# Performance work log

Hardware: AMD Instinct MI355X
Metric: run time of the kernel (lower is better)

The kernel has to match this reference:

```python
import jax, jax.numpy as jnp
import numpy as np

B, L, H, O, T = 64, 128, 1024, 1, 256


def setup_inputs() -> dict:
    key = jax.random.key(0)
    ks = jax.random.split(key, 9)
    s = 1.0 / np.sqrt(H)
    return {
        "latent": jax.random.normal(ks[0], (B, L), dtype=jnp.float32),
        "W_lin": jax.random.normal(ks[1], (H, L), dtype=jnp.float32) / np.sqrt(L),
        "b_lin": jax.random.normal(ks[2], (H,), dtype=jnp.float32) * 0.01,
        "W_ih": jax.random.normal(ks[3], (4 * H, H), dtype=jnp.float32) * s,
        "W_hh": jax.random.normal(ks[4], (4 * H, H), dtype=jnp.float32) * s,
        "b_ih": jax.random.normal(ks[5], (4 * H,), dtype=jnp.float32) * s,
        "b_hh": jax.random.normal(ks[6], (4 * H,), dtype=jnp.float32) * s,
        "W_out": jax.random.normal(ks[7], (O, H), dtype=jnp.float32) / np.sqrt(H),
        "b_out": jax.random.normal(ks[8], (O,), dtype=jnp.float32) * 0.01,
        "seq_len": T,
    }


def reference(latent, W_lin, b_lin, W_ih, W_hh, b_ih, b_hh, W_out, b_out, seq_len):
    # latent -> hidden projection: [B, H]
    hidden = latent @ W_lin.T + b_lin
    h_dim = W_hh.shape[1]
    batch = hidden.shape[0]
    # Input is identical at every timestep, so the input-to-gate projection
    # is computed once (same math as applying it per step). [B, 4H]
    x_gates = hidden @ W_ih.T + (b_ih + b_hh)

    def step(carry, _):
        h, c = carry
        gates = x_gates + h @ W_hh.T  # [B, 4H]
        i, f, g, o = jnp.split(gates, 4, axis=-1)  # PyTorch gate order i,f,g,o
        i = jax.nn.sigmoid(i)
        f = jax.nn.sigmoid(f)
        g = jnp.tanh(g)
        o = jax.nn.sigmoid(o)
        c = f * c + i * g
        h = o * jnp.tanh(c)
        return (h, c), h

    init = (jnp.zeros((batch, h_dim), hidden.dtype), jnp.zeros((batch, h_dim), hidden.dtype))
    _, hs = jax.lax.scan(step, init, None, length=seq_len)  # [T, B, H]
    decoded = jnp.transpose(hs, (1, 0, 2))  # [B, T, H]
    out = decoded @ W_out.T + b_out  # [B, T, O]
    return out
```

## Files before the change

kernel.cpp:

```cpp
#include <hip/hip_runtime.h>
#include <hip/hip_cooperative_groups.h>

#define B_  64
#define L_  128
#define H_  1024
#define G4_ 4096
#define T_  256
#define NWG 256

typedef __attribute__((ext_vector_type(8))) short bf16x8;
typedef __attribute__((ext_vector_type(4))) float f32x4;

__device__ __forceinline__ float shx(float v, int m) { return __shfl_xor(v, m, 64); }

__device__ __forceinline__ unsigned rne_bf16(float x) {
    unsigned u = __builtin_bit_cast(unsigned, x);
    return (u + 0x7FFFu + ((u >> 16) & 1u)) >> 16;
}
__device__ __forceinline__ float bf16_to_f32(unsigned h) {
    return __builtin_bit_cast(float, h << 16);
}

__global__ void hidden_kernel(const float* __restrict__ latent,
                              const float* __restrict__ W_lin,
                              const float* __restrict__ b_lin,
                              float* __restrict__ hidden) {
    const int wave = (blockIdx.x * blockDim.x + threadIdx.x) >> 6;
    const int lane = threadIdx.x & 63;
    for (int o = 0; o < 64; ++o) {
        const int out = wave * 64 + o;
        const int b = out >> 10, j = out & 1023;
        const float2 wv = *(const float2*)(W_lin + j * L_ + lane * 2);
        const float2 xv = *(const float2*)(latent + b * L_ + lane * 2);
        float p = wv.x * xv.x + wv.y * xv.y;
        #pragma unroll
        for (int m = 1; m < 64; m <<= 1) p += shx(p, m);
        if (lane == 0) hidden[out] = p + b_lin[j];
    }
}

__global__ void xgates_kernel(const float* __restrict__ hidden,
                              const float* __restrict__ W_ih,
                              const float* __restrict__ b_ih,
                              const float* __restrict__ b_hh,
                              float* __restrict__ x_gates) {
    const int wave = (blockIdx.x * blockDim.x + threadIdx.x) >> 6;
    const int lane = threadIdx.x & 63;
    for (int o = 0; o < 64; ++o) {
        const int out = wave * 64 + o;
        const int b = out >> 12, j = out & 4095;
        float p = 0.f;
        #pragma unroll
        for (int q = 0; q < 4; ++q) {
            const float4 wv = *(const float4*)(W_ih + j * H_ + q * 256 + lane * 4);
            const float4 hv = *(const float4*)(hidden + b * H_ + q * 256 + lane * 4);
            p += wv.x * hv.x + wv.y * hv.y + wv.z * hv.z + wv.w * hv.w;
        }
        #pragma unroll
        for (int m = 1; m < 64; m <<= 1) p += shx(p, m);
        if (lane == 0) x_gates[out] = p + b_ih[j] + b_hh[j];
    }
}

__global__ void __launch_bounds__(1024, 4)
lstm_kernel(const float* __restrict__ W_hh,
            const float* __restrict__ x_gates,
            const float* __restrict__ W_out,
            unsigned* __restrict__ h_buf,
            float* __restrict__ part,
            int*   __restrict__ bar)
{
    extern __shared__ float smem[];
    unsigned* Hhi32 = (unsigned*)smem;
    unsigned* Hlo32 = (unsigned*)smem + 8192;
    float*    Gred  = smem + 16384;

    const int tid = threadIdx.x;
    const int l   = tid & 63;
    const int wv  = tid >> 6;
    const int tau = wv & 3;
    const int kq  = wv >> 2;
    const int hs  = blockIdx.x >> 2;
    const int bg  = blockIdx.x & 3;
    const int row16 = l & 15;
    const int kg    = l >> 4;

    bf16x8 Ahi[8], Alo[8];
    {
        const float* wrow = W_hh + (size_t)(tau * H_ + hs * 16 + row16) * H_;
        #pragma unroll
        for (int s = 0; s < 8; ++s) {
            const int ks = kq * 8 + s;
            const float* p = wrow + ks * 32 + kg * 8;
            const float4 f0 = *(const float4*)p;
            const float4 f1 = *(const float4*)(p + 4);
            const float w[8] = {f0.x, f0.y, f0.z, f0.w, f1.x, f1.y, f1.z, f1.w};
            #pragma unroll
            for (int j = 0; j < 8; ++j) {
                const unsigned hb = rne_bf16(w[j]);
                const float lo = w[j] - bf16_to_f32(hb);
                Ahi[s][j] = (short)hb;
                Alo[s][j] = (short)rne_bf16(lo);
            }
        }
    }

    const int bb  = tid >> 4;
    const int hix = tid & 15;
    const int bG  = bg * 16 + bb;
    float xgi = 0, xgf = 0, xgg = 0, xgo = 0, wo = 0;
    if (tid < 256) {
        const float* xg = x_gates + (size_t)bG * G4_ + hs * 16 + hix;
        xgi = xg[0]; xgf = xg[H_]; xgg = xg[2 * H_]; xgo = xg[3 * H_];
        wo  = W_out[hs * 16 + hix];
    }
    float c_state = 0.f;

    int* cnt = bar + bg * 64;
    int* gen = bar + bg * 64 + 32;

    int cur = 0;
    for (int t = 0; t < T_; ++t) {
        {
            const int b = wv;
            const unsigned long long* src =
                (const unsigned long long*)(h_buf + (size_t)cur * (B_ * H_) +
                                            (size_t)(bg * 16 + b) * H_);
            #pragma unroll
            for (int i = 0; i < 8; ++i) {
                const int d = i * 64 + l;
                const unsigned long long v =
                    __hip_atomic_load(src + d, __ATOMIC_RELAXED,
                                      __HIP_MEMORY_SCOPE_AGENT);
                const unsigned p0 = (unsigned)v;
                const unsigned p1 = (unsigned)(v >> 32);
                const int dw = b * 512 + (((d >> 2) ^ (b & 7)) << 2) + (d & 3);
                Hhi32[dw] = (p1 & 0xFFFF0000u) | (p0 >> 16);
                Hlo32[dw] = ((p1 & 0xFFFFu) << 16) | (p0 & 0xFFFFu);
            }
        }
        __syncthreads();

        {
            f32x4 acc = {0.f, 0.f, 0.f, 0.f};
            const char* HhiB = (const char*)smem;
            const char* HloB = (const char*)smem + 32768;
            #pragma unroll
            for (int s = 0; s < 8; ++s) {
                const int ks  = kq * 8 + s;
                const int off = row16 * 2048 + (((ks * 4 + kg) ^ (row16 & 7)) << 4);
                const bf16x8 Bhi = *(const bf16x8*)(HhiB + off);
                const bf16x8 Blo = *(const bf16x8*)(HloB + off);
                acc = __builtin_amdgcn_mfma_f32_16x16x32_bf16(Ahi[s], Bhi, acc, 0, 0, 0);
                acc = __builtin_amdgcn_mfma_f32_16x16x32_bf16(Ahi[s], Blo, acc, 0, 0, 0);
                acc = __builtin_amdgcn_mfma_f32_16x16x32_bf16(Alo[s], Bhi, acc, 0, 0, 0);
            }
            #pragma unroll
            for (int r = 0; r < 4; ++r)
                Gred[((tau * 4 + kq) * 16 + kg * 4 + r) * 17 + row16] = acc[r];
        }
        __syncthreads();

        if (tid < 256) {
            float gs[4];
            #pragma unroll
            for (int g = 0; g < 4; ++g) {
                float s = 0.f;
                #pragma unroll
                for (int q = 0; q < 4; ++q)
                    s += Gred[((g * 4 + q) * 16 + hix) * 17 + bb];
                gs[g] = s;
            }
            const float gi_ = xgi + gs[0];
            const float gf_ = xgf + gs[1];
            const float gg_ = xgg + gs[2];
            const float go_ = xgo + gs[3];
            const float i_ = 1.f / (1.f + expf(-gi_));
            const float f_ = 1.f / (1.f + expf(-gf_));
            const float g_ = tanhf(gg_);
            const float o_ = 1.f / (1.f + expf(-go_));
            c_state = f_ * c_state + i_ * g_;
            const float hv = o_ * tanhf(c_state);
            const unsigned hb = rne_bf16(hv);
            const float lo = hv - bf16_to_f32(hb);
            const unsigned packed = (hb << 16) | rne_bf16(lo);
            __hip_atomic_store(h_buf + (size_t)(cur ^ 1) * (B_ * H_) +
                               (size_t)bG * H_ + hs * 16 + hix,
                               packed, __ATOMIC_RELAXED, __HIP_MEMORY_SCOPE_AGENT);
            float pp = hv * wo;
            pp += shx(pp, 1); pp += shx(pp, 2); pp += shx(pp, 4); pp += shx(pp, 8);
            if (hix == 0) part[((size_t)t * B_ + bG) * 64 + hs] = pp;
        }

        asm volatile("s_waitcnt vmcnt(0)" ::: "memory");
        __syncthreads();
        if (tid == 0) {
            if (__hip_atomic_fetch_add(cnt, 1, __ATOMIC_RELAXED,
                                       __HIP_MEMORY_SCOPE_AGENT) == 64 * (t + 1) - 1) {
                __hip_atomic_store(gen, t + 1, __ATOMIC_RELAXED,
                                   __HIP_MEMORY_SCOPE_AGENT);
            } else {
                while (__hip_atomic_load(gen, __ATOMIC_RELAXED,
                                         __HIP_MEMORY_SCOPE_AGENT) < t + 1) {}
            }
        }
        __syncthreads();
        cur ^= 1;
    }
}

__global__ void out_kernel(const float* __restrict__ part,
                           const float* __restrict__ b_out,
                           float* __restrict__ out) {
    const int g = blockIdx.x * blockDim.x + threadIdx.x;
    const int t = g >> 6, b = g & 63;
    const float4* p4 = (const float4*)(part + ((size_t)t * B_ + b) * 64);
    float s = 0.f;
    #pragma unroll
    for (int i = 0; i < 16; ++i) {
        const float4 v = p4[i];
        s += v.x + v.y + v.z + v.w;
    }
    out[b * T_ + t] = s + b_out[0];
}

extern "C" void kernel_launch(void* const* d_in, const int* in_sizes, int n_in,
                              void* d_out, int out_size, void* d_ws, size_t ws_size,
                              hipStream_t stream) {
    const float* latent = (const float*)d_in[0];
    const float* W_lin  = (const float*)d_in[1];
    const float* b_lin  = (const float*)d_in[2];
    const float* W_ih   = (const float*)d_in[3];
    const float* W_hh   = (const float*)d_in[4];
    const float* b_ih   = (const float*)d_in[5];
    const float* b_hh   = (const float*)d_in[6];
    const float* W_out  = (const float*)d_in[7];
    const float* b_out  = (const float*)d_in[8];

    float* ws      = (float*)d_ws;
    float* hidden  = ws;
    float* x_gates = hidden  + 65536;
    unsigned* h_buf = (unsigned*)(x_gates + 262144);
    float* part    = (float*)(h_buf + 131072);
    int*   bar     = (int*)(part + 1048576);
    float* out     = (float*)d_out;

    hipMemsetAsync(h_buf, 0, (size_t)2 * B_ * H_ * sizeof(unsigned), stream);
    hipMemsetAsync(bar, 0, 4 * 64 * sizeof(int), stream);

    const int lds_bytes = 65536 + 4352 * 4;
    hipFuncSetAttribute((const void*)lstm_kernel,
                        hipFuncAttributeMaxDynamicSharedMemorySize, lds_bytes);

    hidden_kernel<<<256, 256, 0, stream>>>(latent, W_lin, b_lin, hidden);
    xgates_kernel<<<1024, 256, 0, stream>>>(hidden, W_ih, b_ih, b_hh, x_gates);

    void* args[] = { (void*)&W_hh, (void*)&x_gates, (void*)&W_out,
                     (void*)&h_buf, (void*)&part, (void*)&bar };
    hipLaunchCooperativeKernel(reinterpret_cast<void*>(lstm_kernel),
                               dim3(NWG), dim3(1024), args, lds_bytes, stream);

    out_kernel<<<64, 256, 0, stream>>>(part, b_out, out);
}
```

Before: 1.767 ms.

## Replace counter barrier with per-block flags, store raw h in LDS, split gates per wave

```diff
diff --git a/kernel.cpp b/kernel.cpp
--- a/kernel.cpp
+++ b/kernel.cpp
@@ -1,5 +1,4 @@
 #include <hip/hip_runtime.h>
-#include <hip/hip_cooperative_groups.h>
 
 #define B_  64
 #define L_  128
@@ -10,6 +9,7 @@
 
 typedef __attribute__((ext_vector_type(8))) short bf16x8;
 typedef __attribute__((ext_vector_type(4))) float f32x4;
+typedef __attribute__((ext_vector_type(4))) unsigned u32x4;
 
 __device__ __forceinline__ float shx(float v, int m) { return __shfl_xor(v, m, 64); }
 
@@ -46,8 +46,8 @@
                               float* __restrict__ x_gates) {
     const int wave = (blockIdx.x * blockDim.x + threadIdx.x) >> 6;
     const int lane = threadIdx.x & 63;
-    for (int o = 0; o < 64; ++o) {
-        const int out = wave * 64 + o;
+    for (int o = 0; o < 16; ++o) {
+        const int out = wave * 16 + o;
         const int b = out >> 12, j = out & 4095;
         float p = 0.f;
         #pragma unroll
@@ -62,7 +62,7 @@
     }
 }
 
-__global__ void __launch_bounds__(1024, 4)
+__global__ void __launch_bounds__(1024, 2)
 lstm_kernel(const float* __restrict__ W_hh,
             const float* __restrict__ x_gates,
             const float* __restrict__ W_out,
@@ -71,26 +71,27 @@
             int*   __restrict__ bar)
 {
     extern __shared__ float smem[];
-    unsigned* Hhi32 = (unsigned*)smem;
-    unsigned* Hlo32 = (unsigned*)smem + 8192;
-    float*    Gred  = smem + 16384;
+    unsigned* Hraw = (unsigned*)smem;
+    float*    Gred = smem + 16384;
 
     const int tid = threadIdx.x;
     const int l   = tid & 63;
     const int wv  = tid >> 6;
-    const int tau = wv & 3;
-    const int kq  = wv >> 2;
+    const int kq  = wv >> 1;
+    const int tp  = wv & 1;
     const int hs  = blockIdx.x >> 2;
     const int bg  = blockIdx.x & 3;
     const int row16 = l & 15;
     const int kg    = l >> 4;
 
-    bf16x8 Ahi[8], Alo[8];
-    {
-        const float* wrow = W_hh + (size_t)(tau * H_ + hs * 16 + row16) * H_;
-        #pragma unroll
-        for (int s = 0; s < 8; ++s) {
-            const int ks = kq * 8 + s;
+    bf16x8 Ahi[2][4], Alo[2][4];
+    #pragma unroll
+    for (int g = 0; g < 2; ++g) {
+        const int gate = tp * 2 + g;
+        const float* wrow = W_hh + (size_t)(gate * H_ + hs * 16 + row16) * H_;
+        #pragma unroll
+        for (int s = 0; s < 4; ++s) {
+            const int ks = kq * 4 + s;
             const float* p = wrow + ks * 32 + kg * 8;
             const float4 f0 = *(const float4*)p;
             const float4 f1 = *(const float4*)(p + 4);
@@ -99,8 +100,8 @@
             for (int j = 0; j < 8; ++j) {
                 const unsigned hb = rne_bf16(w[j]);
                 const float lo = w[j] - bf16_to_f32(hb);
-                Ahi[s][j] = (short)hb;
-                Alo[s][j] = (short)rne_bf16(lo);
+                Ahi[g][s][j] = (short)hb;
+                Alo[g][s][j] = (short)rne_bf16(lo);
             }
         }
     }
@@ -116,48 +117,56 @@
     }
     float c_state = 0.f;
 
-    int* cnt = bar + bg * 64;
-    int* gen = bar + bg * 64 + 32;
-
+    unsigned long long* H64 = (unsigned long long*)Hraw;
     int cur = 0;
     for (int t = 0; t < T_; ++t) {
         {
-            const int b = wv;
             const unsigned long long* src =
                 (const unsigned long long*)(h_buf + (size_t)cur * (B_ * H_) +
-                                            (size_t)(bg * 16 + b) * H_);
+                                            (size_t)(bg * 16 + wv) * H_);
+            unsigned long long v[8];
+            #pragma unroll
+            for (int i = 0; i < 8; ++i)
+                v[i] = __hip_atomic_load(src + i * 64 + l, __ATOMIC_RELAXED,
+                                         __HIP_MEMORY_SCOPE_AGENT);
             #pragma unroll
             for (int i = 0; i < 8; ++i) {
                 const int d = i * 64 + l;
-                const unsigned long long v =
-                    __hip_atomic_load(src + d, __ATOMIC_RELAXED,
-                                      __HIP_MEMORY_SCOPE_AGENT);
-                const unsigned p0 = (unsigned)v;
-                const unsigned p1 = (unsigned)(v >> 32);
-                const int dw = b * 512 + (((d >> 2) ^ (b & 7)) << 2) + (d & 3);
-                Hhi32[dw] = (p1 & 0xFFFF0000u) | (p0 >> 16);
-                Hlo32[dw] = ((p1 & 0xFFFFu) << 16) | (p0 & 0xFFFFu);
+                H64[wv * 512 + (((d >> 1) ^ (wv & 7)) << 1) + (d & 1)] = v[i];
             }
         }
         __syncthreads();
 
         {
-            f32x4 acc = {0.f, 0.f, 0.f, 0.f};
-            const char* HhiB = (const char*)smem;
-            const char* HloB = (const char*)smem + 32768;
-            #pragma unroll
-            for (int s = 0; s < 8; ++s) {
-                const int ks  = kq * 8 + s;
-                const int off = row16 * 2048 + (((ks * 4 + kg) ^ (row16 & 7)) << 4);
-                const bf16x8 Bhi = *(const bf16x8*)(HhiB + off);
-                const bf16x8 Blo = *(const bf16x8*)(HloB + off);
-                acc = __builtin_amdgcn_mfma_f32_16x16x32_bf16(Ahi[s], Bhi, acc, 0, 0, 0);
-                acc = __builtin_amdgcn_mfma_f32_16x16x32_bf16(Ahi[s], Blo, acc, 0, 0, 0);
-                acc = __builtin_amdgcn_mfma_f32_16x16x32_bf16(Alo[s], Bhi, acc, 0, 0, 0);
-            }
-            #pragma unroll
-            for (int r = 0; r < 4; ++r)
-                Gred[((tau * 4 + kq) * 16 + kg * 4 + r) * 17 + row16] = acc[r];
+            f32x4 acc0 = {0.f, 0.f, 0.f, 0.f};
+            f32x4 acc1 = {0.f, 0.f, 0.f, 0.f};
+            const unsigned* Hb = Hraw + row16 * 1024;
+            const int sw = row16 & 7;
+            #pragma unroll
+            for (int s = 0; s < 4; ++s) {
+                const int g0 = (kq * 4 + s) * 8 + kg * 2;
+                const u32x4 ra = *(const u32x4*)(Hb + ((g0 ^ sw) << 2));
+                const u32x4 rb = *(const u32x4*)(Hb + (((g0 + 1) ^ sw) << 2));
+                u32x4 bh, bl;
+                bh[0] = __builtin_amdgcn_perm(ra[1], ra[0], 0x07060302u);
+                bl[0] = __builtin_amdgcn_perm(ra[1], ra[0], 0x05040100u);
+                bh[1] = __builtin_amdgcn_perm(ra[3], ra[2], 0x07060302u);
+                bl[1] = __builtin_amdgcn_perm(ra[3], ra[2], 0x05040100u);
+                bh[2] = __builtin_amdgcn_perm(rb[1], rb[0], 0x07060302u);
+                bl[2] = __builtin_amdgcn_perm(rb[1], rb[0], 0x05040100u);
+                bh[3] = __builtin_amdgcn_perm(rb[3], rb[2], 0x07060302u);
+                bl[3] = __builtin_amdgcn_perm(rb[3], rb[2], 0x05040100u);
+                const bf16x8 Bhi = __builtin_bit_cast(bf16x8, bh);
+                const bf16x8 Blo = __builtin_bit_cast(bf16x8, bl);
+                acc0 = __builtin_amdgcn_mfma_f32_16x16x32_bf16(Ahi[0][s], Bhi, acc0, 0, 0, 0);
+                acc0 = __builtin_amdgcn_mfma_f32_16x16x32_bf16(Ahi[0][s], Blo, acc0, 0, 0, 0);
+                acc0 = __builtin_amdgcn_mfma_f32_16x16x32_bf16(Alo[0][s], Bhi, acc0, 0, 0, 0);
+                acc1 = __builtin_amdgcn_mfma_f32_16x16x32_bf16(Ahi[1][s], Bhi, acc1, 0, 0, 0);
+                acc1 = __builtin_amdgcn_mfma_f32_16x16x32_bf16(Ahi[1][s], Blo, acc1, 0, 0, 0);
+                acc1 = __builtin_amdgcn_mfma_f32_16x16x32_bf16(Alo[1][s], Bhi, acc1, 0, 0, 0);
+            }
+            *(f32x4*)(Gred + (((tp * 2 + 0) * 8 + kq) * 16 + row16) * 20 + kg * 4) = acc0;
+            *(f32x4*)(Gred + (((tp * 2 + 1) * 8 + kq) * 16 + row16) * 20 + kg * 4) = acc1;
         }
         __syncthreads();
 
@@ -167,8 +176,8 @@
             for (int g = 0; g < 4; ++g) {
                 float s = 0.f;
                 #pragma unroll
-                for (int q = 0; q < 4; ++q)
-                    s += Gred[((g * 4 + q) * 16 + hix) * 17 + bb];
+                for (int q = 0; q < 8; ++q)
+                    s += Gred[((g * 8 + q) * 16 + bb) * 20 + hix];
                 gs[g] = s;
             }
             const float gi_ = xgi + gs[0];
@@ -194,15 +203,14 @@
 
         asm volatile("s_waitcnt vmcnt(0)" ::: "memory");
         __syncthreads();
-        if (tid == 0) {
-            if (__hip_atomic_fetch_add(cnt, 1, __ATOMIC_RELAXED,
-                                       __HIP_MEMORY_SCOPE_AGENT) == 64 * (t + 1) - 1) {
-                __hip_atomic_store(gen, t + 1, __ATOMIC_RELAXED,
-                                   __HIP_MEMORY_SCOPE_AGENT);
-            } else {
-                while (__hip_atomic_load(gen, __ATOMIC_RELAXED,
-                                         __HIP_MEMORY_SCOPE_AGENT) < t + 1) {}
-            }
+        if (tid == 0)
+            __hip_atomic_store(bar + bg * 1024 + hs * 16, t + 1,
+                               __ATOMIC_RELAXED, __HIP_MEMORY_SCOPE_AGENT);
+        if (tid < 64) {
+            const int* sp = bar + bg * 1024 + tid * 16;
+            while (__hip_atomic_load(sp, __ATOMIC_RELAXED,
+                                     __HIP_MEMORY_SCOPE_AGENT) < t + 1)
+                __builtin_amdgcn_s_sleep(1);
         }
         __syncthreads();
         cur ^= 1;
@@ -246,14 +254,14 @@
     float* out     = (float*)d_out;
 
     hipMemsetAsync(h_buf, 0, (size_t)2 * B_ * H_ * sizeof(unsigned), stream);
-    hipMemsetAsync(bar, 0, 4 * 64 * sizeof(int), stream);
-
-    const int lds_bytes = 65536 + 4352 * 4;
+    hipMemsetAsync(bar, 0, 4 * 1024 * sizeof(int), stream);
+
+    const int lds_bytes = (16384 + 4 * 8 * 16 * 20) * sizeof(float);
     hipFuncSetAttribute((const void*)lstm_kernel,
                         hipFuncAttributeMaxDynamicSharedMemorySize, lds_bytes);
 
     hidden_kernel<<<256, 256, 0, stream>>>(latent, W_lin, b_lin, hidden);
-    xgates_kernel<<<1024, 256, 0, stream>>>(hidden, W_ih, b_ih, b_hh, x_gates);
+    xgates_kernel<<<4096, 256, 0, stream>>>(hidden, W_ih, b_ih, b_hh, x_gates);
 
     void* args[] = { (void*)&W_hh, (void*)&x_gates, (void*)&W_out,
                      (void*)&h_buf, (void*)&part, (void*)&bar };
```

New measurement: 1.539 ms. 1.15x faster.
